# Kernel tuning notes

Measured on AMD Instinct MI355X. Metric: run time of the kernel, lower is better.

## Reference

```python
import jax, jax.numpy as jnp
import numpy as np

WIN = 7
NUM_HEADS = 4
DIM = 128
HEAD_DIM = DIM // NUM_HEADS
N = WIN * WIN
NW = 1024   # windows per image (224/7)^2
B_ = 16384  # batch(16) * NW


def _pos_index(win):
    # Swin relative-position index, static int table [N, N]
    coords = np.stack(np.meshgrid(np.arange(win), np.arange(win), indexing='ij'))
    cf = coords.reshape(2, -1)                       # [2, N]
    rel = cf[:, :, None] - cf[:, None, :]            # [2, N, N]
    rel = rel.transpose(1, 2, 0).astype(np.int64)    # [N, N, 2]
    rel[:, :, 0] += win - 1
    rel[:, :, 1] += win - 1
    rel[:, :, 0] *= 2 * win - 1
    return rel.sum(-1)                               # [N, N]

POS_INDEX = jnp.asarray(_pos_index(WIN))


def setup_inputs() -> dict:
    key = jax.random.key(0)
    ks = jax.random.split(key, 11)
    s = 0.02
    return {
        'x': jax.random.normal(ks[0], (B_, N, DIM), jnp.float32),
        'mask': jax.random.normal(ks[1], (NW, N, N), jnp.float32),
        'Wq': jax.random.normal(ks[2], (DIM, DIM), jnp.float32) * s,
        'bq': jax.random.normal(ks[3], (DIM,), jnp.float32) * s,
        'Wk': jax.random.normal(ks[4], (DIM, DIM), jnp.float32) * s,
        'bk': jax.random.normal(ks[5], (DIM,), jnp.float32) * s,
        'Wv': jax.random.normal(ks[6], (DIM, DIM), jnp.float32) * s,
        'bv': jax.random.normal(ks[7], (DIM,), jnp.float32) * s,
        'Wproj': jax.random.normal(ks[8], (DIM, DIM), jnp.float32) * s,
        'bproj': jax.random.normal(ks[9], (DIM,), jnp.float32) * s,
        'rel_bias': jax.random.normal(ks[10], ((2 * WIN - 1) ** 2, NUM_HEADS), jnp.float32) * s,
    }


def reference(x, mask, Wq, bq, Wk, bk, Wv, bv, Wproj, bproj, rel_bias):
    Bw, n, C = x.shape
    H, hd = NUM_HEADS, HEAD_DIM
    scale = hd ** -0.5

    def heads(t):  # [B, N, C] -> [B, H, N, hd]
        return t.reshape(Bw, n, H, hd).transpose(0, 2, 1, 3)

    q = heads(x @ Wq.T + bq) * scale
    k = heads(x @ Wk.T + bk)
    v = heads(x @ Wv.T + bv)

    attn = jnp.einsum('bhnd,bhmd->bhnm', q, k)              # [B, H, N, N]
    rb = rel_bias[POS_INDEX.reshape(-1)].reshape(n, n, H)    # [N, N, H]
    attn = attn + rb.transpose(2, 0, 1)[None]                # + [1, H, N, N]

    nw = mask.shape[0]
    attn = attn.reshape(Bw // nw, nw, H, n, n) + mask[None, :, None]
    attn = attn.reshape(Bw, H, n, n)

    attn = jax.nn.softmax(attn, axis=-1)
    out = jnp.einsum('bhnm,bhmd->bhnd', attn, v)             # [B, H, N, hd]
    out = out.transpose(0, 2, 1, 3).reshape(Bw, n, C)
    return out @ Wproj.T + bproj
```

## Files before the change

### kernel.cpp

```cpp
#include <hip/hip_runtime.h>
#include <hip/hip_bf16.h>
#include <stdint.h>

#define NTOK 49
#define LOG2E 1.4426950408889634f
#define SCALE2 0.25507662683243807f

typedef __attribute__((ext_vector_type(4))) float f32x4;
typedef __attribute__((ext_vector_type(2))) unsigned int u32x2;
typedef __attribute__((ext_vector_type(4))) unsigned int u32x4;
typedef __attribute__((ext_vector_type(8))) short bfrag;
typedef __attribute__((ext_vector_type(4))) short s16x4;
typedef __attribute__((ext_vector_type(4))) float facc;

#define MFMA16(A,B,C) __builtin_amdgcn_mfma_f32_16x16x32_bf16(A,B,C,0,0,0)
#define EXP2(x) __builtin_amdgcn_exp2f(x)

__device__ __forceinline__ unsigned pk2bf(float a, float b) {
    unsigned r;
    asm("v_cvt_pk_bf16_f32 %0, %1, %2" : "=v"(r) : "v"(a), "v"(b));
    return r;
}
__device__ __forceinline__ short f2bf(float a) {
    unsigned ua = __builtin_bit_cast(unsigned, a);
    ua = ua + 0x7fffu + ((ua >> 16) & 1u);
    return (short)(ua >> 16);
}
__device__ __forceinline__ float bf2f(short s) {
    unsigned u = ((unsigned)(unsigned short)s) << 16;
    return __builtin_bit_cast(float, u);
}
__device__ __forceinline__ int sw256(int row, int cb) { return row * 256 + (cb ^ ((row & 7) << 4)); }
__device__ __forceinline__ int sw128(int row, int cb) { return row * 128 + (cb ^ ((row & 7) << 4)); }

__global__ void prep_w(const float* __restrict__ Wq, const float* __restrict__ Wk,
                       const float* __restrict__ Wv, const float* __restrict__ Wp,
                       const float* __restrict__ relb, short* __restrict__ ws)
{
    int t = blockIdx.x * 256 + threadIdx.x;
    if (t >= 16384) return;
    int e = t & 7, lane = (t >> 3) & 63, ks = (t >> 9) & 3, tile = t >> 11;
    int row = tile * 16 + (lane & 15);
    int col = ks * 32 + (lane >> 4) * 8 + e;
    int src = row * 128 + col;
    ws[t]         = f2bf(Wq[src]);
    ws[16384 + t] = f2bf(Wk[src]);
    ws[32768 + t] = f2bf(Wv[src]);
    ws[49152 + t] = f2bf(Wp[src]);
    int e2 = t & 3, lane2 = (t >> 2) & 63, mt = (t >> 8) & 3, rt = (t >> 10) & 3, h = t >> 12;
    int r = rt * 16 + (lane2 & 15);
    int m = mt * 16 + (lane2 >> 4) * 4 + e2;
    float v = 0.f;
    if (r < NTOK && m < NTOK) {
        int idx = ((r / 7 - m / 7) + 6) * 13 + ((r % 7) - (m % 7) + 6);
        v = relb[idx * 4 + h] * LOG2E;
    }
    ws[65536 + t] = f2bf(v);
}

__global__ void prep_cmb(const float* __restrict__ mask, const float* __restrict__ relb,
                         short* __restrict__ cmb)
{
    int t = blockIdx.x * 256 + threadIdx.x;
    int e = t & 3, lane = (t >> 2) & 63, mt = (t >> 8) & 3, rt = (t >> 10) & 3;
    int h = (t >> 12) & 3, w = t >> 14;
    int r = rt * 16 + (lane & 15);
    int m = mt * 16 + (lane >> 4) * 4 + e;
    float v = -1e30f;
    if (r < NTOK && m < NTOK) {
        int idx = ((r / 7 - m / 7) + 6) * 13 + ((r % 7) - (m % 7) + 6);
        v = (mask[w * (NTOK * NTOK) + r * NTOK + m] + relb[idx * 4 + h]) * LOG2E;
    }
    cmb[t] = f2bf(v);
}

__device__ __forceinline__ char* pstrip(char* smem_, int wid, int r, int mb) {
    return smem_ + ((mb >> 6) << 14) + r * 256 + ((wid * 64 + (mb & 63)) ^ ((r & 7) << 4));
}

__global__ __launch_bounds__(256, 2) void swin_fwd_p(
    const float* __restrict__ x,
    const float* __restrict__ bq, const float* __restrict__ bk,
    const float* __restrict__ bv, const float* __restrict__ bp,
    const short* __restrict__ wqf, const short* __restrict__ wkf,
    const short* __restrict__ wvf, const short* __restrict__ wpf,
    const short* __restrict__ cmbf, float* __restrict__ out)
{
    extern __shared__ char smem[];
    char* qbuf  = smem;
    char* kbuf  = smem + 16384;
    char* vtbuf = smem + 32768;
    char* r4    = smem + 49152;

    const int b = blockIdx.x;
    const int tid = threadIdx.x;
    const int wid = tid >> 6;
    const int lane = tid & 63;
    const int l16 = lane & 15;
    const int lg = lane >> 4;

    float bqv[2][4], bkv[2][4], bpv[2][4], bvv2[2];
    #pragma unroll
    for (int mt = 0; mt < 2; ++mt) {
        #pragma unroll
        for (int j = 0; j < 4; ++j) {
            int o = wid * 32 + mt * 16 + lg * 4 + j;
            bqv[mt][j] = bq[o]; bkv[mt][j] = bk[o]; bpv[mt][j] = bp[o];
        }
        bvv2[mt] = bv[wid * 32 + mt * 16 + l16];
    }

    bfrag aq[2][4], ak[2][4], av[2][4];
    {
        const short* wq_i = wqf; const short* wk_i = wkf; const short* wv_i = wvf;
        asm volatile("" : "+s"(wq_i), "+s"(wk_i), "+s"(wv_i));
        #pragma unroll
        for (int mt = 0; mt < 2; ++mt)
            #pragma unroll
            for (int ks = 0; ks < 4; ++ks) {
                int fi = (((wid * 2 + mt) * 4 + ks) * 64 + lane) * 8;
                aq[mt][ks] = *(const bfrag*)(wq_i + fi);
                ak[mt][ks] = *(const bfrag*)(wk_i + fi);
                av[mt][ks] = *(const bfrag*)(wv_i + fi);
            }
    }

    f32x4 xr[7];
    {
        const float* xw0 = x + (size_t)b * 6272;
        #pragma unroll
        for (int ii = 0; ii < 7; ++ii) {
            int i4 = ii * 256 + tid;
            if (i4 < 1568) xr[ii] = *(const f32x4*)(xw0 + i4 * 4);
        }
        #pragma unroll
        for (int ii = 0; ii < 7; ++ii) {
            int i4 = ii * 256 + tid;
            if (i4 < 1568) {
                int tok = i4 >> 5, col = (i4 & 31) * 4;
                u32x2 w; w.x = pk2bf(xr[ii].x, xr[ii].y); w.y = pk2bf(xr[ii].z, xr[ii].w);
                *(u32x2*)(r4 + sw256(tok, col * 2)) = w;
            }
        }
        if (tid < 240) { u32x4 z = {0, 0, 0, 0}; *(u32x4*)(r4 + 49 * 256 + tid * 16) = z; }
    }
    __syncthreads();

    #pragma unroll 1
    for (int it = 0; it < 32; ++it) {
        const int win = b + (it << 9);

        {
            const float* xn = x + (size_t)((win + 512) & 16383) * 6272;
            #pragma unroll
            for (int ii = 0; ii < 7; ++ii) {
                int i4 = ii * 256 + tid;
                if (i4 < 1568) xr[ii] = *(const f32x4*)(xn + i4 * 4);
            }
        }

        {
            #pragma unroll
            for (int nt = 0; nt < 4; ++nt) {
                bfrag bx[4];
                #pragma unroll
                for (int ks = 0; ks < 4; ++ks)
                    bx[ks] = *(const bfrag*)(r4 + sw256(nt * 16 + l16, (ks * 32 + lg * 8) * 2));
                facc accq[2] = {{0,0,0,0},{0,0,0,0}};
                facc acck[2] = {{0,0,0,0},{0,0,0,0}};
                facc accv[2] = {{0,0,0,0},{0,0,0,0}};
                __builtin_amdgcn_s_setprio(1);
                #pragma unroll
                for (int ks = 0; ks < 4; ++ks)
                    #pragma unroll
                    for (int mt = 0; mt < 2; ++mt) {
                        accq[mt] = MFMA16(aq[mt][ks], bx[ks], accq[mt]);
                        acck[mt] = MFMA16(ak[mt][ks], bx[ks], acck[mt]);
                        accv[mt] = MFMA16(bx[ks], av[mt][ks], accv[mt]);
                    }
                __builtin_amdgcn_s_setprio(0);
                int tok = nt * 16 + l16;
                #pragma unroll
                for (int mt = 0; mt < 2; ++mt) {
                    int o0 = wid * 32 + mt * 16 + lg * 4;
                    u32x2 wq2, wk2, wv2;
                    wq2.x = pk2bf((accq[mt][0] + bqv[mt][0]) * SCALE2, (accq[mt][1] + bqv[mt][1]) * SCALE2);
                    wq2.y = pk2bf((accq[mt][2] + bqv[mt][2]) * SCALE2, (accq[mt][3] + bqv[mt][3]) * SCALE2);
                    wk2.x = pk2bf(acck[mt][0] + bkv[mt][0], acck[mt][1] + bkv[mt][1]);
                    wk2.y = pk2bf(acck[mt][2] + bkv[mt][2], acck[mt][3] + bkv[mt][3]);
                    *(u32x2*)(qbuf + sw256(tok, o0 * 2)) = wq2;
                    *(u32x2*)(kbuf + sw256(tok, o0 * 2)) = wk2;
                    wv2.x = pk2bf(accv[mt][0] + bvv2[mt], accv[mt][1] + bvv2[mt]);
                    wv2.y = pk2bf(accv[mt][2] + bvv2[mt], accv[mt][3] + bvv2[mt]);
                    *(u32x2*)(vtbuf + sw128(wid * 32 + mt * 16 + l16, (nt * 16 + lg * 4) * 2)) = wv2;
                }
            }
        }

        facc s[4][4];
        {
            bfrag ka[4], qb[4];
            int cb = (wid * 32 + lg * 8) * 2;
            #pragma unroll
            for (int t = 0; t < 4; ++t) {
                ka[t] = *(const bfrag*)(kbuf + sw256(t * 16 + l16, cb));
                qb[t] = *(const bfrag*)(qbuf + sw256(t * 16 + l16, cb));
            }
            __builtin_amdgcn_s_setprio(1);
            #pragma unroll
            for (int mt = 0; mt < 4; ++mt)
                #pragma unroll
                for (int rt = 0; rt < 4; ++rt) {
                    facc z = {0, 0, 0, 0};
                    s[mt][rt] = MFMA16(ka[mt], qb[rt], z);
                }
            __builtin_amdgcn_s_setprio(0);
        }
        __syncthreads();

        {
            #pragma unroll
            for (int ii = 0; ii < 7; ++ii) {
                int i4 = ii * 256 + tid;
                if (i4 < 1568) {
                    int tok = i4 >> 5, col = (i4 & 31) * 4;
                    u32x2 w; w.x = pk2bf(xr[ii].x, xr[ii].y); w.y = pk2bf(xr[ii].z, xr[ii].w);
                    *(u32x2*)(r4 + sw256(tok, col * 2)) = w;
                }
            }
        }

        float rs4[4];
        {
            const short* cw = cmbf + ((size_t)((win & 1023) * 4 + wid) << 12);
            #pragma unroll
            for (int rt = 0; rt < 4; ++rt) {
                float lgt[4][4];
                float mx = -3e38f;
                #pragma unroll
                for (int mt = 0; mt < 4; ++mt) {
                    s16x4 b4 = *(const s16x4*)(cw + ((rt * 4 + mt) << 8) + lane * 4);
                    #pragma unroll
                    for (int j = 0; j < 4; ++j) {
                        float v = s[mt][rt][j] + bf2f(b4[j]);
                        lgt[mt][j] = v;
                        mx = fmaxf(mx, v);
                    }
                }
                mx = fmaxf(mx, __shfl_xor(mx, 16));
                mx = fmaxf(mx, __shfl_xor(mx, 32));
                float sum = 0.f;
                u32x2 pw[4];
                #pragma unroll
                for (int mt = 0; mt < 4; ++mt) {
                    float p0 = EXP2(lgt[mt][0] - mx);
                    float p1 = EXP2(lgt[mt][1] - mx);
                    float p2 = EXP2(lgt[mt][2] - mx);
                    float p3 = EXP2(lgt[mt][3] - mx);
                    sum += (p0 + p1) + (p2 + p3);
                    pw[mt].x = pk2bf(p0, p1);
                    pw[mt].y = pk2bf(p2, p3);
                }
                sum += __shfl_xor(sum, 16);
                sum += __shfl_xor(sum, 32);
                rs4[rt] = __builtin_amdgcn_rcpf(sum);
                int r = rt * 16 + l16;
                #pragma unroll
                for (int mt = 0; mt < 4; ++mt)
                    *(u32x2*)pstrip(smem, wid, r, mt * 32 + lg * 8) = pw[mt];
            }
        }

        facc o2[2][4];
        {
            #pragma unroll
            for (int ct = 0; ct < 2; ++ct)
                #pragma unroll
                for (int rt = 0; rt < 4; ++rt) o2[ct][rt] = (facc){0, 0, 0, 0};
            #pragma unroll
            for (int ks = 0; ks < 2; ++ks) {
                bfrag avf[2], pb[4];
                #pragma unroll
                for (int ct = 0; ct < 2; ++ct)
                    avf[ct] = *(const bfrag*)(vtbuf + sw128(wid * 32 + ct * 16 + l16, (ks * 32 + lg * 8) * 2));
                #pragma unroll
                for (int rt = 0; rt < 4; ++rt)
                    pb[rt] = *(const bfrag*)pstrip(smem, wid, rt * 16 + l16, ks * 64 + lg * 16);
                __builtin_amdgcn_s_setprio(1);
                #pragma unroll
                for (int ct = 0; ct < 2; ++ct)
                    #pragma unroll
                    for (int rt = 0; rt < 4; ++rt)
                        o2[ct][rt] = MFMA16(avf[ct], pb[rt], o2[ct][rt]);
                __builtin_amdgcn_s_setprio(0);
            }
        }
        bfrag ap[2][4];
        {
            const short* wp_i = wpf;
            asm volatile("" : "+s"(wp_i));
            #pragma unroll
            for (int mt = 0; mt < 2; ++mt)
                #pragma unroll
                for (int ks = 0; ks < 4; ++ks)
                    ap[mt][ks] = *(const bfrag*)(wp_i + (((wid * 2 + mt) * 4 + ks) * 64 + lane) * 8);
        }
        __syncthreads();
        {
            #pragma unroll
            for (int ct = 0; ct < 2; ++ct) {
                int c0 = wid * 32 + ct * 16 + lg * 4;
                #pragma unroll
                for (int rt = 0; rt < 4; ++rt) {
                    int r = rt * 16 + l16;
                    float sc = rs4[rt];
                    u32x2 w;
                    w.x = pk2bf(o2[ct][rt][0] * sc, o2[ct][rt][1] * sc);
                    w.y = pk2bf(o2[ct][rt][2] * sc, o2[ct][rt][3] * sc);
                    *(u32x2*)(qbuf + sw256(r, c0 * 2)) = w;
                }
            }
        }
        __syncthreads();

        {
            facc acco[2][4];
            #pragma unroll
            for (int mt = 0; mt < 2; ++mt)
                #pragma unroll
                for (int tt = 0; tt < 4; ++tt) acco[mt][tt] = (facc){0, 0, 0, 0};
            #pragma unroll
            for (int tt = 0; tt < 4; ++tt) {
                bfrag ba[4];
                #pragma unroll
                for (int ks = 0; ks < 4; ++ks)
                    ba[ks] = *(const bfrag*)(qbuf + sw256(tt * 16 + l16, (ks * 32 + lg * 8) * 2));
                __builtin_amdgcn_s_setprio(1);
                #pragma unroll
                for (int ks = 0; ks < 4; ++ks)
                    #pragma unroll
                    for (int mt = 0; mt < 2; ++mt)
                        acco[mt][tt] = MFMA16(ap[mt][ks], ba[ks], acco[mt][tt]);
                __builtin_amdgcn_s_setprio(0);
            }
            float* ow = out + (size_t)win * 6272;
            #pragma unroll
            for (int tt = 0; tt < 4; ++tt) {
                int tok = tt * 16 + l16;
                if (tok < NTOK) {
                    #pragma unroll
                    for (int mt = 0; mt < 2; ++mt) {
                        int o0 = wid * 32 + mt * 16 + lg * 4;
                        f32x4 w;
                        w.x = acco[mt][tt][0] + bpv[mt][0];
                        w.y = acco[mt][tt][1] + bpv[mt][1];
                        w.z = acco[mt][tt][2] + bpv[mt][2];
                        w.w = acco[mt][tt][3] + bpv[mt][3];
                        *(f32x4*)(ow + tok * 128 + o0) = w;
                    }
                }
            }
        }

        {
            const short* wq_i = wqf; const short* wk_i = wkf; const short* wv_i = wvf;
            asm volatile("" : "+s"(wq_i), "+s"(wk_i), "+s"(wv_i));
            #pragma unroll
            for (int mt = 0; mt < 2; ++mt)
                #pragma unroll
                for (int ks = 0; ks < 4; ++ks) {
                    int fi = (((wid * 2 + mt) * 4 + ks) * 64 + lane) * 8;
                    aq[mt][ks] = *(const bfrag*)(wq_i + fi);
                    ak[mt][ks] = *(const bfrag*)(wk_i + fi);
                    av[mt][ks] = *(const bfrag*)(wv_i + fi);
                }
        }
        __syncthreads();
    }
}

__global__ __launch_bounds__(256, 2) void swin_fwd_fb(
    const float* __restrict__ x, const float* __restrict__ mask,
    const float* __restrict__ bq, const float* __restrict__ bk,
    const float* __restrict__ bv, const float* __restrict__ bp,
    const short* __restrict__ wqf, const short* __restrict__ wkf,
    const short* __restrict__ wvf, const short* __restrict__ wpf,
    const short* __restrict__ rbf, float* __restrict__ out)
{
    extern __shared__ char smem[];
    char* qbuf  = smem;
    char* kbuf  = smem + 16384;
    char* vtbuf = smem + 32768;
    char* r4    = smem + 49152;

    const int win = blockIdx.x;
    const int tid = threadIdx.x;
    const int wid = tid >> 6;
    const int lane = tid & 63;
    const int l16 = lane & 15;
    const int lg = lane >> 4;

    {
        const float* xw = x + (size_t)win * 6272;
        #pragma unroll
        for (int i = 0; i < 7; ++i) {
            int i4 = i * 256 + tid;
            if (i4 < 1568) {
                f32x4 f = *(const f32x4*)(xw + i4 * 4);
                int tok = i4 >> 5, col = (i4 & 31) * 4;
                u32x2 w; w.x = pk2bf(f.x, f.y); w.y = pk2bf(f.z, f.w);
                *(u32x2*)(r4 + sw256(tok, col * 2)) = w;
            }
        }
        if (tid < 240) { u32x4 z = {0, 0, 0, 0}; *(u32x4*)(r4 + 49 * 256 + tid * 16) = z; }
    }
    bfrag aq[2][4], ak[2][4], av[2][4];
    float bqv[2][4], bkv[2][4], bvv2[2];
    #pragma unroll
    for (int mt = 0; mt < 2; ++mt) {
        #pragma unroll
        for (int ks = 0; ks < 4; ++ks) {
            int fi = (((wid * 2 + mt) * 4 + ks) * 64 + lane) * 8;
            aq[mt][ks] = *(const bfrag*)(wqf + fi);
            ak[mt][ks] = *(const bfrag*)(wkf + fi);
            av[mt][ks] = *(const bfrag*)(wvf + fi);
        }
        #pragma unroll
        for (int j = 0; j < 4; ++j) {
            int o = wid * 32 + mt * 16 + lg * 4 + j;
            bqv[mt][j] = bq[o]; bkv[mt][j] = bk[o];
        }
        bvv2[mt] = bv[wid * 32 + mt * 16 + l16];
    }
    __syncthreads();

    {
        #pragma unroll
        for (int nt = 0; nt < 4; ++nt) {
            bfrag bx[4];
            #pragma unroll
            for (int ks = 0; ks < 4; ++ks)
                bx[ks] = *(const bfrag*)(r4 + sw256(nt * 16 + l16, (ks * 32 + lg * 8) * 2));
            facc accq[2] = {{0,0,0,0},{0,0,0,0}};
            facc acck[2] = {{0,0,0,0},{0,0,0,0}};
            facc accv[2] = {{0,0,0,0},{0,0,0,0}};
            #pragma unroll
            for (int ks = 0; ks < 4; ++ks)
                #pragma unroll
                for (int mt = 0; mt < 2; ++mt) {
                    accq[mt] = MFMA16(aq[mt][ks], bx[ks], accq[mt]);
                    acck[mt] = MFMA16(ak[mt][ks], bx[ks], acck[mt]);
                    accv[mt] = MFMA16(bx[ks], av[mt][ks], accv[mt]);
                }
            int tok = nt * 16 + l16;
            #pragma unroll
            for (int mt = 0; mt < 2; ++mt) {
                int o0 = wid * 32 + mt * 16 + lg * 4;
                u32x2 wq2, wk2, wv2;
                wq2.x = pk2bf((accq[mt][0] + bqv[mt][0]) * SCALE2, (accq[mt][1] + bqv[mt][1]) * SCALE2);
                wq2.y = pk2bf((accq[mt][2] + bqv[mt][2]) * SCALE2, (accq[mt][3] + bqv[mt][3]) * SCALE2);
                wk2.x = pk2bf(acck[mt][0] + bkv[mt][0], acck[mt][1] + bkv[mt][1]);
                wk2.y = pk2bf(acck[mt][2] + bkv[mt][2], acck[mt][3] + bkv[mt][3]);
                *(u32x2*)(qbuf + sw256(tok, o0 * 2)) = wq2;
                *(u32x2*)(kbuf + sw256(tok, o0 * 2)) = wk2;
                wv2.x = pk2bf(accv[mt][0] + bvv2[mt], accv[mt][1] + bvv2[mt]);
                wv2.y = pk2bf(accv[mt][2] + bvv2[mt], accv[mt][3] + bvv2[mt]);
                *(u32x2*)(vtbuf + sw128(wid * 32 + mt * 16 + l16, (nt * 16 + lg * 4) * 2)) = wv2;
            }
        }
    }
    facc s[4][4];
    {
        bfrag ka[4], qb[4];
        int cb = (wid * 32 + lg * 8) * 2;
        #pragma unroll
        for (int t = 0; t < 4; ++t) {
            ka[t] = *(const bfrag*)(kbuf + sw256(t * 16 + l16, cb));
            qb[t] = *(const bfrag*)(qbuf + sw256(t * 16 + l16, cb));
        }
        #pragma unroll
        for (int mt = 0; mt < 4; ++mt)
            #pragma unroll
            for (int rt = 0; rt < 4; ++rt) {
                facc z = {0, 0, 0, 0};
                s[mt][rt] = MFMA16(ka[mt], qb[rt], z);
            }
    }
    __syncthreads();
    {
        const float* mw = mask + (size_t)(win & 1023) * (NTOK * NTOK);
        #pragma unroll
        for (int i = 0; i < 16; ++i) {
            int flat = i * 256 + tid;
            int r = flat >> 6, m = flat & 63;
            float v = -1e30f;
            if (r < NTOK && m < NTOK) v = mw[r * 49 + m] * LOG2E;
            *(float*)(r4 + sw256(r, m * 4)) = v;
        }
    }
    __syncthreads();
    float rs4[4];
    {
        #pragma unroll
        for (int rt = 0; rt < 4; ++rt) {
            int r = rt * 16 + l16;
            float lgt[4][4];
            float mx = -3e38f;
            #pragma unroll
            for (int mt = 0; mt < 4; ++mt) {
                s16x4 b4 = *(const s16x4*)(rbf + ((wid * 16 + rt * 4 + mt) * 64 + lane) * 4);
                f32x4 mk = *(const f32x4*)(r4 + sw256(r, (mt * 16 + lg * 4) * 4));
                #pragma unroll
                for (int j = 0; j < 4; ++j) {
                    float v = s[mt][rt][j] + bf2f(b4[j]) + mk[j];
                    lgt[mt][j] = v;
                    mx = fmaxf(mx, v);
                }
            }
            mx = fmaxf(mx, __shfl_xor(mx, 16));
            mx = fmaxf(mx, __shfl_xor(mx, 32));
            float sum = 0.f;
            u32x2 pw[4];
            #pragma unroll
            for (int mt = 0; mt < 4; ++mt) {
                float p0 = EXP2(lgt[mt][0] - mx);
                float p1 = EXP2(lgt[mt][1] - mx);
                float p2 = EXP2(lgt[mt][2] - mx);
                float p3 = EXP2(lgt[mt][3] - mx);
                sum += (p0 + p1) + (p2 + p3);
                pw[mt].x = pk2bf(p0, p1);
                pw[mt].y = pk2bf(p2, p3);
            }
            sum += __shfl_xor(sum, 16);
            sum += __shfl_xor(sum, 32);
            rs4[rt] = __builtin_amdgcn_rcpf(sum);
            #pragma unroll
            for (int mt = 0; mt < 4; ++mt)
                *(u32x2*)pstrip(smem, wid, r, mt * 32 + lg * 8) = pw[mt];
        }
    }
    facc o2[2][4];
    {
        #pragma unroll
        for (int ct = 0; ct < 2; ++ct)
            #pragma unroll
            for (int rt = 0; rt < 4; ++rt) o2[ct][rt] = (facc){0, 0, 0, 0};
        #pragma unroll
        for (int ks = 0; ks < 2; ++ks) {
            bfrag avf[2], pb[4];
            #pragma unroll
            for (int ct = 0; ct < 2; ++ct)
                avf[ct] = *(const bfrag*)(vtbuf + sw128(wid * 32 + ct * 16 + l16, (ks * 32 + lg * 8) * 2));
            #pragma unroll
            for (int rt = 0; rt < 4; ++rt)
                pb[rt] = *(const bfrag*)pstrip(smem, wid, rt * 16 + l16, ks * 64 + lg * 16);
            #pragma unroll
            for (int ct = 0; ct < 2; ++ct)
                #pragma unroll
                for (int rt = 0; rt < 4; ++rt)
                    o2[ct][rt] = MFMA16(avf[ct], pb[rt], o2[ct][rt]);
        }
    }
    bfrag ap[2][4];
    float bpv[2][4];
    #pragma unroll
    for (int mt = 0; mt < 2; ++mt) {
        #pragma unroll
        for (int ks = 0; ks < 4; ++ks)
            ap[mt][ks] = *(const bfrag*)(wpf + (((wid * 2 + mt) * 4 + ks) * 64 + lane) * 8);
        #pragma unroll
        for (int j = 0; j < 4; ++j)
            bpv[mt][j] = bp[wid * 32 + mt * 16 + lg * 4 + j];
    }
    __syncthreads();
    {
        #pragma unroll
        for (int ct = 0; ct < 2; ++ct) {
            int c0 = wid * 32 + ct * 16 + lg * 4;
            #pragma unroll
            for (int rt = 0; rt < 4; ++rt) {
                int r = rt * 16 + l16;
                float sc = rs4[rt];
                u32x2 w;
                w.x = pk2bf(o2[ct][rt][0] * sc, o2[ct][rt][1] * sc);
                w.y = pk2bf(o2[ct][rt][2] * sc, o2[ct][rt][3] * sc);
                *(u32x2*)(r4 + sw256(r, c0 * 2)) = w;
            }
        }
    }
    __syncthreads();
    {
        facc acco[2][4];
        #pragma unroll
        for (int mt = 0; mt < 2; ++mt)
            #pragma unroll
            for (int tt = 0; tt < 4; ++tt) acco[mt][tt] = (facc){0, 0, 0, 0};
        #pragma unroll
        for (int tt = 0; tt < 4; ++tt) {
            bfrag ba[4];
            #pragma unroll
            for (int ks = 0; ks < 4; ++ks)
                ba[ks] = *(const bfrag*)(r4 + sw256(tt * 16 + l16, (ks * 32 + lg * 8) * 2));
            #pragma unroll
            for (int ks = 0; ks < 4; ++ks)
                #pragma unroll
                for (int mt = 0; mt < 2; ++mt)
                    acco[mt][tt] = MFMA16(ap[mt][ks], ba[ks], acco[mt][tt]);
        }
        float* ow = out + (size_t)win * 6272;
        #pragma unroll
        for (int tt = 0; tt < 4; ++tt) {
            int tok = tt * 16 + l16;
            if (tok < NTOK) {
                #pragma unroll
                for (int mt = 0; mt < 2; ++mt) {
                    int o0 = wid * 32 + mt * 16 + lg * 4;
                    f32x4 w;
                    w.x = acco[mt][tt][0] + bpv[mt][0];
                    w.y = acco[mt][tt][1] + bpv[mt][1];
                    w.z = acco[mt][tt][2] + bpv[mt][2];
                    w.w = acco[mt][tt][3] + bpv[mt][3];
                    *(f32x4*)(ow + tok * 128 + o0) = w;
                }
            }
        }
    }
}

extern "C" void kernel_launch(void* const* d_in, const int* in_sizes, int n_in,
                              void* d_out, int out_size, void* d_ws, size_t ws_size,
                              hipStream_t stream)
{
    const float* x    = (const float*)d_in[0];
    const float* mask = (const float*)d_in[1];
    const float* Wq   = (const float*)d_in[2];
    const float* bq   = (const float*)d_in[3];
    const float* Wk   = (const float*)d_in[4];
    const float* bk   = (const float*)d_in[5];
    const float* Wv   = (const float*)d_in[6];
    const float* bv   = (const float*)d_in[7];
    const float* Wp   = (const float*)d_in[8];
    const float* bp   = (const float*)d_in[9];
    const float* rlb  = (const float*)d_in[10];
    short* ws = (short*)d_ws;
    short* cmb = ws + 81920;
    const size_t need = ((size_t)81920 + (size_t)16777216) * 2;
    const bool use_cmb = ws_size >= need;

    prep_w<<<64, 256, 0, stream>>>(Wq, Wk, Wv, Wp, rlb, ws);
    if (use_cmb) {
        prep_cmb<<<65536, 256, 0, stream>>>(mask, rlb, cmb);
        swin_fwd_p<<<512, 256, 65536, stream>>>(x, bq, bk, bv, bp,
            ws, ws + 16384, ws + 32768, ws + 49152, cmb, (float*)d_out);
    } else {
        swin_fwd_fb<<<16384, 256, 65536, stream>>>(x, mask, bq, bk, bv, bp,
            ws, ws + 16384, ws + 32768, ws + 49152, ws + 65536, (float*)d_out);
    }
}
```

Before: 370.6 us.

## Shrink shared memory to per-wave scratch and run three blocks per CU

Replaces the shared Q/K/V^T buffers with a small per-wave scratch region, since each wave owns one head. This cuts LDS use from 64KB to 48KB so that three blocks fit per CU, and the persistent grid grows from 512 to 768 blocks with an uneven per-block window count. K is kept in registers and written over Q in scratch after Q fragments are read, and P is split into two halves so the PV MFMA runs in two passes. The mask/bias loads are hoisted before the QK MFMAs and the next-window x prefetch is moved later to overlap with compute. These changes raise register pressure and add more LDS round trips per wave.

```diff
diff --git a/kernel.cpp b/kernel.cpp
--- a/kernel.cpp
+++ b/kernel.cpp
@@ -31,7 +31,8 @@
     return __builtin_bit_cast(float, u);
 }
 __device__ __forceinline__ int sw256(int row, int cb) { return row * 256 + (cb ^ ((row & 7) << 4)); }
-__device__ __forceinline__ int sw128(int row, int cb) { return row * 128 + (cb ^ ((row & 7) << 4)); }
+__device__ __forceinline__ int strip64(int row, int cb) { return row * 64 + (cb ^ (((row >> 1) & 3) << 4)); }
+__device__ __forceinline__ int sw128v(int row, int cb) { return row * 128 + (cb ^ ((row & 7) << 4)); }
 
 __global__ void prep_w(const float* __restrict__ Wq, const float* __restrict__ Wk,
                        const float* __restrict__ Wv, const float* __restrict__ Wp,
@@ -74,11 +75,7 @@
     cmb[t] = f2bf(v);
 }
 
-__device__ __forceinline__ char* pstrip(char* smem_, int wid, int r, int mb) {
-    return smem_ + ((mb >> 6) << 14) + r * 256 + ((wid * 64 + (mb & 63)) ^ ((r & 7) << 4));
-}
-
-__global__ __launch_bounds__(256, 2) void swin_fwd_p(
+__global__ __launch_bounds__(256, 3) void swin_fwd_p(
     const float* __restrict__ x,
     const float* __restrict__ bq, const float* __restrict__ bk,
     const float* __restrict__ bv, const float* __restrict__ bp,
@@ -87,10 +84,8 @@
     const short* __restrict__ cmbf, float* __restrict__ out)
 {
     extern __shared__ char smem[];
-    char* qbuf  = smem;
-    char* kbuf  = smem + 16384;
-    char* vtbuf = smem + 32768;
-    char* r4    = smem + 49152;
+    char* xbuf = smem;
+    char* attb = smem + 16384;
 
     const int b = blockIdx.x;
     const int tid = threadIdx.x;
@@ -98,6 +93,8 @@
     const int lane = tid & 63;
     const int l16 = lane & 15;
     const int lg = lane >> 4;
+    char* wscr = smem + 16384 + wid * 8192;
+    const int cnt = (b < 256) ? 22 : 21;
 
     float bqv[2][4], bkv[2][4], bpv[2][4], bvv2[2];
     #pragma unroll
@@ -139,33 +136,25 @@
             if (i4 < 1568) {
                 int tok = i4 >> 5, col = (i4 & 31) * 4;
                 u32x2 w; w.x = pk2bf(xr[ii].x, xr[ii].y); w.y = pk2bf(xr[ii].z, xr[ii].w);
-                *(u32x2*)(r4 + sw256(tok, col * 2)) = w;
-            }
-        }
-        if (tid < 240) { u32x4 z = {0, 0, 0, 0}; *(u32x4*)(r4 + 49 * 256 + tid * 16) = z; }
+                *(u32x2*)(xbuf + sw256(tok, col * 2)) = w;
+            }
+        }
+        if (tid < 240) { u32x4 z = {0, 0, 0, 0}; *(u32x4*)(xbuf + 49 * 256 + tid * 16) = z; }
     }
     __syncthreads();
 
     #pragma unroll 1
-    for (int it = 0; it < 32; ++it) {
-        const int win = b + (it << 9);
-
-        {
-            const float* xn = x + (size_t)((win + 512) & 16383) * 6272;
-            #pragma unroll
-            for (int ii = 0; ii < 7; ++ii) {
-                int i4 = ii * 256 + tid;
-                if (i4 < 1568) xr[ii] = *(const f32x4*)(xn + i4 * 4);
-            }
-        }
-
+    for (int it = 0; it < cnt; ++it) {
+        const int win = b + it * 768;
+
+        u32x2 kp[4][2];
         {
             #pragma unroll
             for (int nt = 0; nt < 4; ++nt) {
                 bfrag bx[4];
                 #pragma unroll
                 for (int ks = 0; ks < 4; ++ks)
-                    bx[ks] = *(const bfrag*)(r4 + sw256(nt * 16 + l16, (ks * 32 + lg * 8) * 2));
+                    bx[ks] = *(const bfrag*)(xbuf + sw256(nt * 16 + l16, (ks * 32 + lg * 8) * 2));
                 facc accq[2] = {{0,0,0,0},{0,0,0,0}};
                 facc acck[2] = {{0,0,0,0},{0,0,0,0}};
                 facc accv[2] = {{0,0,0,0},{0,0,0,0}};
@@ -182,30 +171,44 @@
                 int tok = nt * 16 + l16;
                 #pragma unroll
                 for (int mt = 0; mt < 2; ++mt) {
-                    int o0 = wid * 32 + mt * 16 + lg * 4;
-                    u32x2 wq2, wk2, wv2;
+                    u32x2 wq2, wv2;
                     wq2.x = pk2bf((accq[mt][0] + bqv[mt][0]) * SCALE2, (accq[mt][1] + bqv[mt][1]) * SCALE2);
                     wq2.y = pk2bf((accq[mt][2] + bqv[mt][2]) * SCALE2, (accq[mt][3] + bqv[mt][3]) * SCALE2);
-                    wk2.x = pk2bf(acck[mt][0] + bkv[mt][0], acck[mt][1] + bkv[mt][1]);
-                    wk2.y = pk2bf(acck[mt][2] + bkv[mt][2], acck[mt][3] + bkv[mt][3]);
-                    *(u32x2*)(qbuf + sw256(tok, o0 * 2)) = wq2;
-                    *(u32x2*)(kbuf + sw256(tok, o0 * 2)) = wk2;
+                    *(u32x2*)(wscr + strip64(tok, mt * 32 + lg * 8)) = wq2;
+                    kp[nt][mt].x = pk2bf(acck[mt][0] + bkv[mt][0], acck[mt][1] + bkv[mt][1]);
+                    kp[nt][mt].y = pk2bf(acck[mt][2] + bkv[mt][2], acck[mt][3] + bkv[mt][3]);
                     wv2.x = pk2bf(accv[mt][0] + bvv2[mt], accv[mt][1] + bvv2[mt]);
                     wv2.y = pk2bf(accv[mt][2] + bvv2[mt], accv[mt][3] + bvv2[mt]);
-                    *(u32x2*)(vtbuf + sw128(wid * 32 + mt * 16 + l16, (nt * 16 + lg * 4) * 2)) = wv2;
-                }
-            }
+                    *(u32x2*)(wscr + 4096 + sw128v(mt * 16 + l16, nt * 32 + lg * 8)) = wv2;
+                }
+            }
+        }
+        bfrag qb[4];
+        #pragma unroll
+        for (int t = 0; t < 4; ++t)
+            qb[t] = *(const bfrag*)(wscr + strip64(t * 16 + l16, lg * 16));
+        #pragma unroll
+        for (int nt = 0; nt < 4; ++nt)
+            #pragma unroll
+            for (int mt = 0; mt < 2; ++mt)
+                *(u32x2*)(wscr + strip64(nt * 16 + l16, mt * 32 + lg * 8)) = kp[nt][mt];
+        bfrag ka[4];
+        #pragma unroll
+        for (int t = 0; t < 4; ++t)
+            ka[t] = *(const bfrag*)(wscr + strip64(t * 16 + l16, lg * 16));
+
+        s16x4 b4r[4][4];
+        {
+            const short* cw = cmbf + ((size_t)((win & 1023) * 4 + wid) << 12);
+            #pragma unroll
+            for (int rt = 0; rt < 4; ++rt)
+                #pragma unroll
+                for (int mt = 0; mt < 4; ++mt)
+                    b4r[rt][mt] = *(const s16x4*)(cw + ((rt * 4 + mt) << 8) + lane * 4);
         }
 
         facc s[4][4];
         {
-            bfrag ka[4], qb[4];
-            int cb = (wid * 32 + lg * 8) * 2;
-            #pragma unroll
-            for (int t = 0; t < 4; ++t) {
-                ka[t] = *(const bfrag*)(kbuf + sw256(t * 16 + l16, cb));
-                qb[t] = *(const bfrag*)(qbuf + sw256(t * 16 + l16, cb));
-            }
             __builtin_amdgcn_s_setprio(1);
             #pragma unroll
             for (int mt = 0; mt < 4; ++mt)
@@ -216,37 +219,31 @@
                 }
             __builtin_amdgcn_s_setprio(0);
         }
-        __syncthreads();
-
-        {
+
+        if (it + 1 < cnt) {
+            const float* xn = x + (size_t)(win + 768) * 6272;
             #pragma unroll
             for (int ii = 0; ii < 7; ++ii) {
                 int i4 = ii * 256 + tid;
-                if (i4 < 1568) {
-                    int tok = i4 >> 5, col = (i4 & 31) * 4;
-                    u32x2 w; w.x = pk2bf(xr[ii].x, xr[ii].y); w.y = pk2bf(xr[ii].z, xr[ii].w);
-                    *(u32x2*)(r4 + sw256(tok, col * 2)) = w;
-                }
+                if (i4 < 1568) xr[ii] = *(const f32x4*)(xn + i4 * 4);
             }
         }
 
         float rs4[4];
-        {
-            const short* cw = cmbf + ((size_t)((win & 1023) * 4 + wid) << 12);
+        u32x2 pwB[4][2];
+        {
             #pragma unroll
             for (int rt = 0; rt < 4; ++rt) {
                 float lgt[4][4];
                 float mx = -3e38f;
                 #pragma unroll
-                for (int mt = 0; mt < 4; ++mt) {
-                    s16x4 b4 = *(const s16x4*)(cw + ((rt * 4 + mt) << 8) + lane * 4);
+                for (int mt = 0; mt < 4; ++mt)
                     #pragma unroll
                     for (int j = 0; j < 4; ++j) {
-                        float v = s[mt][rt][j] + bf2f(b4[j]);
+                        float v = s[mt][rt][j] + bf2f(b4r[rt][mt][j]);
                         lgt[mt][j] = v;
                         mx = fmaxf(mx, v);
                     }
-                }
                 mx = fmaxf(mx, __shfl_xor(mx, 16));
                 mx = fmaxf(mx, __shfl_xor(mx, 32));
                 float sum = 0.f;
@@ -265,36 +262,64 @@
                 sum += __shfl_xor(sum, 32);
                 rs4[rt] = __builtin_amdgcn_rcpf(sum);
                 int r = rt * 16 + l16;
-                #pragma unroll
-                for (int mt = 0; mt < 4; ++mt)
-                    *(u32x2*)pstrip(smem, wid, r, mt * 32 + lg * 8) = pw[mt];
+                *(u32x2*)(wscr + strip64(r, lg * 8)) = pw[0];
+                *(u32x2*)(wscr + strip64(r, 32 + lg * 8)) = pw[1];
+                pwB[rt][0] = pw[2]; pwB[rt][1] = pw[3];
             }
         }
 
         facc o2[2][4];
-        {
+        #pragma unroll
+        for (int ct = 0; ct < 2; ++ct)
+            #pragma unroll
+            for (int rt = 0; rt < 4; ++rt) o2[ct][rt] = (facc){0, 0, 0, 0};
+        {
+            bfrag avf[2], pb[4];
             #pragma unroll
             for (int ct = 0; ct < 2; ++ct)
-                #pragma unroll
-                for (int rt = 0; rt < 4; ++rt) o2[ct][rt] = (facc){0, 0, 0, 0};
-            #pragma unroll
-            for (int ks = 0; ks < 2; ++ks) {
-                bfrag avf[2], pb[4];
-                #pragma unroll
-                for (int ct = 0; ct < 2; ++ct)
-                    avf[ct] = *(const bfrag*)(vtbuf + sw128(wid * 32 + ct * 16 + l16, (ks * 32 + lg * 8) * 2));
+                avf[ct] = *(const bfrag*)(wscr + 4096 + sw128v(ct * 16 + l16, lg * 16));
+            #pragma unroll
+            for (int rt = 0; rt < 4; ++rt)
+                pb[rt] = *(const bfrag*)(wscr + strip64(rt * 16 + l16, lg * 16));
+            __builtin_amdgcn_s_setprio(1);
+            #pragma unroll
+            for (int ct = 0; ct < 2; ++ct)
                 #pragma unroll
                 for (int rt = 0; rt < 4; ++rt)
-                    pb[rt] = *(const bfrag*)pstrip(smem, wid, rt * 16 + l16, ks * 64 + lg * 16);
-                __builtin_amdgcn_s_setprio(1);
-                #pragma unroll
-                for (int ct = 0; ct < 2; ++ct)
-                    #pragma unroll
-                    for (int rt = 0; rt < 4; ++rt)
-                        o2[ct][rt] = MFMA16(avf[ct], pb[rt], o2[ct][rt]);
-                __builtin_amdgcn_s_setprio(0);
-            }
-        }
+                    o2[ct][rt] = MFMA16(avf[ct], pb[rt], o2[ct][rt]);
+            __builtin_amdgcn_s_setprio(0);
+        }
+        #pragma unroll
+        for (int rt = 0; rt < 4; ++rt) {
+            int r = rt * 16 + l16;
+            *(u32x2*)(wscr + strip64(r, lg * 8)) = pwB[rt][0];
+            *(u32x2*)(wscr + strip64(r, 32 + lg * 8)) = pwB[rt][1];
+        }
+        {
+            bfrag avf[2], pb[4];
+            #pragma unroll
+            for (int ct = 0; ct < 2; ++ct)
+                avf[ct] = *(const bfrag*)(wscr + 4096 + sw128v(ct * 16 + l16, 64 + lg * 16));
+            #pragma unroll
+            for (int rt = 0; rt < 4; ++rt)
+                pb[rt] = *(const bfrag*)(wscr + strip64(rt * 16 + l16, lg * 16));
+            __builtin_amdgcn_s_setprio(1);
+            #pragma unroll
+            for (int ct = 0; ct < 2; ++ct)
+                #pragma unroll
+                for (int rt = 0; rt < 4; ++rt)
+                    o2[ct][rt] = MFMA16(avf[ct], pb[rt], o2[ct][rt]);
+            __builtin_amdgcn_s_setprio(0);
+        }
+        u32x2 attw[2][4];
+        #pragma unroll
+        for (int ct = 0; ct < 2; ++ct)
+            #pragma unroll
+            for (int rt = 0; rt < 4; ++rt) {
+                float sc = rs4[rt];
+                attw[ct][rt].x = pk2bf(o2[ct][rt][0] * sc, o2[ct][rt][1] * sc);
+                attw[ct][rt].y = pk2bf(o2[ct][rt][2] * sc, o2[ct][rt][3] * sc);
+            }
         bfrag ap[2][4];
         {
             const short* wp_i = wpf;
@@ -306,18 +331,19 @@
                     ap[mt][ks] = *(const bfrag*)(wp_i + (((wid * 2 + mt) * 4 + ks) * 64 + lane) * 8);
         }
         __syncthreads();
-        {
-            #pragma unroll
-            for (int ct = 0; ct < 2; ++ct) {
-                int c0 = wid * 32 + ct * 16 + lg * 4;
-                #pragma unroll
-                for (int rt = 0; rt < 4; ++rt) {
-                    int r = rt * 16 + l16;
-                    float sc = rs4[rt];
-                    u32x2 w;
-                    w.x = pk2bf(o2[ct][rt][0] * sc, o2[ct][rt][1] * sc);
-                    w.y = pk2bf(o2[ct][rt][2] * sc, o2[ct][rt][3] * sc);
-                    *(u32x2*)(qbuf + sw256(r, c0 * 2)) = w;
+        #pragma unroll
+        for (int ct = 0; ct < 2; ++ct)
+            #pragma unroll
+            for (int rt = 0; rt < 4; ++rt)
+                *(u32x2*)(attb + sw256(rt * 16 + l16, (wid * 32 + ct * 16 + lg * 4) * 2)) = attw[ct][rt];
+        if (it + 1 < cnt) {
+            #pragma unroll
+            for (int ii = 0; ii < 7; ++ii) {
+                int i4 = ii * 256 + tid;
+                if (i4 < 1568) {
+                    int tok = i4 >> 5, col = (i4 & 31) * 4;
+                    u32x2 w; w.x = pk2bf(xr[ii].x, xr[ii].y); w.y = pk2bf(xr[ii].z, xr[ii].w);
+                    *(u32x2*)(xbuf + sw256(tok, col * 2)) = w;
                 }
             }
         }
@@ -334,7 +360,7 @@
                 bfrag ba[4];
                 #pragma unroll
                 for (int ks = 0; ks < 4; ++ks)
-                    ba[ks] = *(const bfrag*)(qbuf + sw256(tt * 16 + l16, (ks * 32 + lg * 8) * 2));
+                    ba[ks] = *(const bfrag*)(attb + sw256(tt * 16 + l16, (ks * 32 + lg * 8) * 2));
                 __builtin_amdgcn_s_setprio(1);
                 #pragma unroll
                 for (int ks = 0; ks < 4; ++ks)
@@ -361,7 +387,6 @@
                 }
             }
         }
-
         {
             const short* wq_i = wqf; const short* wk_i = wkf; const short* wv_i = wvf;
             asm volatile("" : "+s"(wq_i), "+s"(wk_i), "+s"(wv_i));
@@ -465,7 +490,7 @@
                 *(u32x2*)(kbuf + sw256(tok, o0 * 2)) = wk2;
                 wv2.x = pk2bf(accv[mt][0] + bvv2[mt], accv[mt][1] + bvv2[mt]);
                 wv2.y = pk2bf(accv[mt][2] + bvv2[mt], accv[mt][3] + bvv2[mt]);
-                *(u32x2*)(vtbuf + sw128(wid * 32 + mt * 16 + l16, (nt * 16 + lg * 4) * 2)) = wv2;
+                *(u32x2*)(vtbuf + sw128v(wid * 32 + mt * 16 + l16, (nt * 16 + lg * 4) * 2)) = wv2;
             }
         }
     }
@@ -535,8 +560,10 @@
             sum += __shfl_xor(sum, 32);
             rs4[rt] = __builtin_amdgcn_rcpf(sum);
             #pragma unroll
-            for (int mt = 0; mt < 4; ++mt)
-                *(u32x2*)pstrip(smem, wid, r, mt * 32 + lg * 8) = pw[mt];
+            for (int mt = 0; mt < 4; ++mt) {
+                int mb = mt * 32 + lg * 8;
+                *(u32x2*)(smem + ((mb >> 6) << 14) + r * 256 + ((wid * 64 + (mb & 63)) ^ ((r & 7) << 4))) = pw[mt];
+            }
         }
     }
     facc o2[2][4];
@@ -550,10 +577,12 @@
             bfrag avf[2], pb[4];
             #pragma unroll
             for (int ct = 0; ct < 2; ++ct)
-                avf[ct] = *(const bfrag*)(vtbuf + sw128(wid * 32 + ct * 16 + l16, (ks * 32 + lg * 8) * 2));
-            #pragma unroll
-            for (int rt = 0; rt < 4; ++rt)
-                pb[rt] = *(const bfrag*)pstrip(smem, wid, rt * 16 + l16, ks * 64 + lg * 16);
+                avf[ct] = *(const bfrag*)(vtbuf + sw128v(wid * 32 + ct * 16 + l16, (ks * 32 + lg * 8) * 2));
+            #pragma unroll
+            for (int rt = 0; rt < 4; ++rt) {
+                int mb = ks * 64 + lg * 16, r = rt * 16 + l16;
+                pb[rt] = *(const bfrag*)(smem + ((mb >> 6) << 14) + r * 256 + ((wid * 64 + (mb & 63)) ^ ((r & 7) << 4)));
+            }
             #pragma unroll
             for (int ct = 0; ct < 2; ++ct)
                 #pragma unroll
@@ -650,7 +679,7 @@
     prep_w<<<64, 256, 0, stream>>>(Wq, Wk, Wv, Wp, rlb, ws);
     if (use_cmb) {
         prep_cmb<<<65536, 256, 0, stream>>>(mask, rlb, cmb);
-        swin_fwd_p<<<512, 256, 65536, stream>>>(x, bq, bk, bv, bp,
+        swin_fwd_p<<<768, 256, 49152, stream>>>(x, bq, bk, bv, bp,
             ws, ws + 16384, ws + 32768, ws + 49152, cmb, (float*)d_out);
     } else {
         swin_fwd_fb<<<16384, 256, 65536, stream>>>(x, mask, bq, bk, bv, bp,
```

New measurement: 801.5 us. +116.3%, slower.
